# Kernel tuning notes

Measured on AMD Instinct MI355X. Metric: run time of the kernel, lower is better.

## Reference

```python
import jax, jax.numpy as jnp
import numpy as np

HEADS = 8
DIM_HEAD = 32
SCALE = DIM_HEAD ** -0.5


def _split_heads(t):
    # [b, n, h*d] -> [b, h, n, d]
    b, n, hd = t.shape
    return t.reshape(b, n, HEADS, hd // HEADS).transpose(0, 2, 1, 3)


def setup_inputs() -> dict:
    key = jax.random.key(0)
    k1, k2, k3, k4 = jax.random.split(key, 4)
    b, n, dim = 2, 2048, 256
    inner = HEADS * DIM_HEAD  # 256
    x = jax.random.normal(k1, (b, n, dim), dtype=jnp.float32)
    attn_feat = jax.random.normal(k2, (b, n, dim), dtype=jnp.float32)
    # nn.Linear(dim, 3*inner, bias=False): store as [dim, 3*inner] for x @ W
    W_qkv = jax.random.normal(k3, (dim, 3 * inner), dtype=jnp.float32) * (dim ** -0.5)
    W_qkv_aux = jax.random.normal(k4, (dim, 3 * inner), dtype=jnp.float32) * (dim ** -0.5)
    return {"x": x, "attn_feat": attn_feat, "W_qkv": W_qkv, "W_qkv_aux": W_qkv_aux,
            "use_cls_tokens": 1}


def reference(x, attn_feat, W_qkv, W_qkv_aux, use_cls_tokens):
    b, n, dim = x.shape
    # aux Q,K (v_aux computed but unused, matching original chunk of 3)
    qkv_aux = attn_feat @ W_qkv_aux            # [b, n, 3*inner]
    q_aux, k_aux, _ = jnp.split(qkv_aux, 3, axis=-1)
    q_aux, k_aux = _split_heads(q_aux), _split_heads(k_aux)
    # self Q,K
    qkv_self = x @ W_qkv
    q_self, k_self, _ = jnp.split(qkv_self, 3, axis=-1)
    q_self, k_self = _split_heads(q_self), _split_heads(k_self)
    # dual score product: (QK^T_aux * scale) * (QK^T_self * scale)
    dots_aux = jnp.einsum('bhid,bhjd->bhij', q_aux, k_aux) * SCALE
    dots_self = jnp.einsum('bhid,bhjd->bhij', q_self, k_self) * SCALE
    attn = jax.nn.softmax(dots_aux * dots_self, axis=-1)  # [b, h, n, n]
    # v = x.unsqueeze(1): broadcast raw x over heads
    out = jnp.einsum('bhij,bjd->bhid', attn, x)           # [b, h, n, dim]
    out = out.transpose(0, 2, 1, 3).reshape(b, n, HEADS * dim)
    attn_flat = attn.transpose(0, 2, 1, 3).reshape(b, n, HEADS * n)
    return (out, out[:, 0], attn_flat[:, 0])
```

## Files before the change

### kernel.cpp

```cpp
#include <hip/hip_runtime.h>

typedef _Float16 f16;
typedef _Float16 f16x4 __attribute__((ext_vector_type(4)));
typedef _Float16 f16x8 __attribute__((ext_vector_type(8)));
typedef float f32x4 __attribute__((ext_vector_type(4)));

#define LOG2E 1.4426950408889634f

__global__ __launch_bounds__(256) void k_transpose(const float* __restrict__ x,
                                                   f16* __restrict__ xt) {
  __shared__ f16 tile[64][65];
  int n0 = blockIdx.x * 64;
  int d0 = blockIdx.y * 64;
  int b  = blockIdx.z;
  int t = threadIdx.x;
  int colr = t & 63, rowg = t >> 6;
#pragma unroll
  for (int r = 0; r < 16; ++r) {
    int row = r * 4 + rowg;
    tile[row][colr] = (f16)x[(b * 2048 + n0 + row) * 256 + d0 + colr];
  }
  __syncthreads();
#pragma unroll
  for (int r = 0; r < 16; ++r) {
    int drow = r * 4 + rowg;
    xt[(b * 256 + d0 + drow) * 2048 + n0 + colr] = tile[colr][drow];
  }
}

__global__ __launch_bounds__(256) void k_proj(const float* __restrict__ x,
    const float* __restrict__ af, const float* __restrict__ Wq,
    const float* __restrict__ Wa, f16* __restrict__ Qs, f16* __restrict__ Ks,
    f16* __restrict__ Qa, f16* __restrict__ Ka) {
  __shared__ f16 Alds[64][264];
  __shared__ f16 Wlds[64][264];
  int mt = blockIdx.x, nt = blockIdx.y, s = blockIdx.z;
  const float* A = s ? af : x;
  const float* W = s ? Wa : Wq;
  f16* Qd = s ? Qa : Qs;
  f16* Kd = s ? Ka : Ks;
  int t = threadIdx.x;
  int m0 = mt * 64, n0 = nt * 64;
  {
    int row = t >> 2, cb = (t & 3) * 64;
    const float* src = A + (m0 + row) * 256 + cb;
#pragma unroll
    for (int r = 0; r < 16; ++r) {
      float4 v = *(const float4*)(src + r * 4);
      f16x4 hv = { (f16)v.x, (f16)v.y, (f16)v.z, (f16)v.w };
      *(f16x4*)&Alds[row][cb + r * 4] = hv;
    }
  }
  {
    int k0 = t >> 4, c4 = (t & 15) * 4;
#pragma unroll
    for (int r = 0; r < 16; ++r) {
      int k = k0 + r * 16;
      float4 v = *(const float4*)(W + k * 768 + n0 + c4);
      Wlds[c4 + 0][k] = (f16)v.x;
      Wlds[c4 + 1][k] = (f16)v.y;
      Wlds[c4 + 2][k] = (f16)v.z;
      Wlds[c4 + 3][k] = (f16)v.w;
    }
  }
  __syncthreads();
  int wv = t >> 6, ln = t & 63, cl = ln & 15, g = ln >> 4;
  f32x4 z4 = {0.f, 0.f, 0.f, 0.f};
  f32x4 acc[4] = {z4, z4, z4, z4};
#pragma unroll
  for (int k32 = 0; k32 < 8; ++k32) {
    f16x8 a = *(const f16x8*)&Alds[wv * 16 + cl][k32 * 32 + g * 8];
#pragma unroll
    for (int n4 = 0; n4 < 4; ++n4) {
      f16x8 bf = *(const f16x8*)&Wlds[n4 * 16 + cl][k32 * 32 + g * 8];
      acc[n4] = __builtin_amdgcn_mfma_f32_16x16x32_f16(a, bf, acc[n4], 0, 0, 0);
    }
  }
#pragma unroll
  for (int n4 = 0; n4 < 4; ++n4) {
    int c = n0 + n4 * 16 + cl;
    int head = (c & 255) >> 5, d = c & 31;
    f16* dst = (c < 256) ? Qd : Kd;
#pragma unroll
    for (int r = 0; r < 4; ++r) {
      int m = m0 + wv * 16 + g * 4 + r;
      int bb = m >> 11, nn = m & 2047;
      dst[((bb * 8 + head) * 2048 + nn) * 32 + d] = (f16)acc[n4][r];
    }
  }
}

__global__ __launch_bounds__(256, 2) void k_flash(const f16* __restrict__ Qs,
    const f16* __restrict__ Ks, const f16* __restrict__ Qa,
    const f16* __restrict__ Ka, const f16* __restrict__ xt,
    float* __restrict__ out, float* __restrict__ out_cls) {
  __shared__ f16 KaL[64][40];
  __shared__ f16 KsL[64][40];
  __shared__ f16 XtL[256][72];
  __shared__ f16 PL[4][16][72];
  int qt = blockIdx.x, h = blockIdx.y, b = blockIdx.z;
  int bh = b * 8 + h;
  int t = threadIdx.x, wv = t >> 6, ln = t & 63, cl = ln & 15, g = ln >> 4;
  int qrow0 = qt * 64 + wv * 16;
  f16x8 qsf = *(const f16x8*)&Qs[(bh * 2048 + qrow0 + cl) * 32 + g * 8];
  f16x8 qaf = *(const f16x8*)&Qa[(bh * 2048 + qrow0 + cl) * 32 + g * 8];
  f32x4 z4 = {0.f, 0.f, 0.f, 0.f};
  f32x4 acc[16];
#pragma unroll
  for (int i = 0; i < 16; ++i) acc[i] = z4;
  float m_run = -__builtin_inff(), l_run = 0.f;
  int krow = t >> 2, koff = (t & 3) * 8;
  const f16* kaSrc = Ka + (bh * 2048 + krow) * 32 + koff;
  const f16* ksSrc = Ks + (bh * 2048 + krow) * 32 + koff;
  const f16* xsrc = xt + (b * 256 + t) * 2048;

  for (int kt = 0; kt < 32; ++kt) {
    __syncthreads();
    *(f16x8*)&KaL[krow][koff] = *(const f16x8*)(kaSrc + kt * 64 * 32);
    *(f16x8*)&KsL[krow][koff] = *(const f16x8*)(ksSrc + kt * 64 * 32);
    {
      const f16* sx = xsrc + kt * 64;
      f16x8* drow = (f16x8*)&XtL[t][0];
#pragma unroll
      for (int r = 0; r < 8; ++r) drow[r] = *(const f16x8*)(sx + r * 8);
    }
    __syncthreads();
    float p[16];
    float tmax = -__builtin_inff();
#pragma unroll
    for (int jt = 0; jt < 4; ++jt) {
      f16x8 kaf = *(const f16x8*)&KaL[jt * 16 + cl][g * 8];
      f16x8 ksf = *(const f16x8*)&KsL[jt * 16 + cl][g * 8];
      f32x4 za = __builtin_amdgcn_mfma_f32_16x16x32_f16(kaf, qaf, z4, 0, 0, 0);
      f32x4 zs = __builtin_amdgcn_mfma_f32_16x16x32_f16(ksf, qsf, z4, 0, 0, 0);
#pragma unroll
      for (int r = 0; r < 4; ++r) {
        float sv = za[r] * zs[r] * (1.f / 32.f);
        p[jt * 4 + r] = sv;
        tmax = fmaxf(tmax, sv);
      }
    }
    tmax = fmaxf(tmax, __shfl_xor(tmax, 16, 64));
    tmax = fmaxf(tmax, __shfl_xor(tmax, 32, 64));
    float m_new = fmaxf(m_run, tmax);
    float alpha = exp2f((m_run - m_new) * LOG2E);
    float lsum = 0.f;
#pragma unroll
    for (int q = 0; q < 16; ++q) {
      p[q] = exp2f((p[q] - m_new) * LOG2E);
      lsum += p[q];
    }
    lsum += __shfl_xor(lsum, 16, 64);
    lsum += __shfl_xor(lsum, 32, 64);
    l_run = l_run * alpha + lsum;
    m_run = m_new;
    float af4[4];
#pragma unroll
    for (int r = 0; r < 4; ++r) af4[r] = __shfl(alpha, g * 4 + r, 64);
#pragma unroll
    for (int dt = 0; dt < 16; ++dt)
#pragma unroll
      for (int r = 0; r < 4; ++r) acc[dt][r] *= af4[r];
#pragma unroll
    for (int jt = 0; jt < 4; ++jt) {
      f16x4 pk = { (f16)p[jt * 4 + 0], (f16)p[jt * 4 + 1],
                   (f16)p[jt * 4 + 2], (f16)p[jt * 4 + 3] };
      *(f16x4*)&PL[wv][cl][jt * 16 + g * 4] = pk;
    }
#pragma unroll
    for (int k32 = 0; k32 < 2; ++k32) {
      f16x8 pf = *(const f16x8*)&PL[wv][cl][k32 * 32 + g * 8];
#pragma unroll
      for (int dt = 0; dt < 16; ++dt) {
        f16x8 xf = *(const f16x8*)&XtL[dt * 16 + cl][k32 * 32 + g * 8];
        acc[dt] = __builtin_amdgcn_mfma_f32_16x16x32_f16(pf, xf, acc[dt], 0, 0, 0);
      }
    }
  }
  float lf[4];
#pragma unroll
  for (int r = 0; r < 4; ++r) lf[r] = __shfl(l_run, g * 4 + r, 64);
#pragma unroll
  for (int dt = 0; dt < 16; ++dt) {
    int col = h * 256 + dt * 16 + cl;
#pragma unroll
    for (int r = 0; r < 4; ++r) {
      int qrow = qrow0 + g * 4 + r;
      float v = acc[dt][r] / lf[r];
      out[(b * 2048 + qrow) * 2048 + col] = v;
      if (qrow == 0) out_cls[b * 2048 + col] = v;
    }
  }
}

__global__ __launch_bounds__(256) void k_attn0(const f16* __restrict__ Qs,
    const f16* __restrict__ Ks, const f16* __restrict__ Qa,
    const f16* __restrict__ Ka, float* __restrict__ dst) {
  __shared__ float qa_s[32], qs_s[32];
  __shared__ float red[256];
  int h = blockIdx.x, b = blockIdx.y, bh = b * 8 + h;
  int t = threadIdx.x;
  if (t < 32) {
    qa_s[t] = (float)Qa[bh * 2048 * 32 + t];
    qs_s[t] = (float)Qs[bh * 2048 * 32 + t];
  }
  __syncthreads();
  float sv[8];
#pragma unroll
  for (int r = 0; r < 8; ++r) {
    int j = r * 256 + t;
    const f16x8* ka8 = (const f16x8*)&Ka[(bh * 2048 + j) * 32];
    const f16x8* ks8 = (const f16x8*)&Ks[(bh * 2048 + j) * 32];
    float da = 0.f, ds = 0.f;
#pragma unroll
    for (int c = 0; c < 4; ++c) {
      f16x8 va = ka8[c], vs = ks8[c];
#pragma unroll
      for (int d = 0; d < 8; ++d) {
        da += qa_s[c * 8 + d] * (float)va[d];
        ds += qs_s[c * 8 + d] * (float)vs[d];
      }
    }
    sv[r] = da * ds * (1.f / 32.f);
  }
  float mx = sv[0];
#pragma unroll
  for (int r = 1; r < 8; ++r) mx = fmaxf(mx, sv[r]);
  red[t] = mx;
  __syncthreads();
  for (int st = 128; st > 0; st >>= 1) {
    if (t < st) red[t] = fmaxf(red[t], red[t + st]);
    __syncthreads();
  }
  float m = red[0];
  __syncthreads();
  float e[8], sum = 0.f;
#pragma unroll
  for (int r = 0; r < 8; ++r) {
    e[r] = exp2f((sv[r] - m) * LOG2E);
    sum += e[r];
  }
  red[t] = sum;
  __syncthreads();
  for (int st = 128; st > 0; st >>= 1) {
    if (t < st) red[t] += red[t + st];
    __syncthreads();
  }
  float l = red[0];
#pragma unroll
  for (int r = 0; r < 8; ++r)
    dst[b * 16384 + h * 2048 + r * 256 + t] = e[r] / l;
}

extern "C" void kernel_launch(void* const* d_in, const int* in_sizes, int n_in,
                              void* d_out, int out_size, void* d_ws, size_t ws_size,
                              hipStream_t stream) {
  const float* x  = (const float*)d_in[0];
  const float* af = (const float*)d_in[1];
  const float* Wq = (const float*)d_in[2];
  const float* Wa = (const float*)d_in[3];
  const size_t QK = (size_t)2 * 8 * 2048 * 32;
  f16* Qs = (f16*)d_ws;
  f16* Ks = Qs + QK;
  f16* Qa = Ks + QK;
  f16* Ka = Qa + QK;
  f16* xt = Ka + QK;
  float* out     = (float*)d_out;
  float* out_cls = out + (size_t)2 * 2048 * 2048;
  float* attn0   = out_cls + 2 * 2048;

  k_transpose<<<dim3(32, 4, 2), 256, 0, stream>>>(x, xt);
  k_proj<<<dim3(64, 8, 2), 256, 0, stream>>>(x, af, Wq, Wa, Qs, Ks, Qa, Ka);
  k_flash<<<dim3(32, 8, 2), 256, 0, stream>>>(Qs, Ks, Qa, Ka, xt, out, out_cls);
  k_attn0<<<dim3(8, 2), 256, 0, stream>>>(Qs, Ks, Qa, Ka, attn0);
}
```

Measured before the change: 200.9 us.

## Restructure flash kernel to split output columns across waves and pre-transpose weights

The flash kernel no longer stages x^T in shared memory. Each wave now owns 64 output columns for all 64 query rows and loads its x^T fragments directly from global memory, with the probabilities shared through LDS. K tiles are double-buffered and prefetched, the log2e factor is folded into the score scale, and accumulator rescaling is skipped when no row max changed. The projection kernel reads a pre-transposed f16 weight produced by a new kernel, plus A straight from global, with no LDS staging. The trade is one extra launch and more global traffic per block for x^T, in exchange for less LDS use and fewer barriers.

```diff
diff --git a/kernel.cpp b/kernel.cpp
--- a/kernel.cpp
+++ b/kernel.cpp
@@ -6,6 +6,7 @@
 typedef float f32x4 __attribute__((ext_vector_type(4)));
 
 #define LOG2E 1.4426950408889634f
+#define SCL   (1.4426950408889634f / 32.0f)
 
 __global__ __launch_bounds__(256) void k_transpose(const float* __restrict__ x,
                                                    f16* __restrict__ xt) {
@@ -18,61 +19,60 @@
 #pragma unroll
   for (int r = 0; r < 16; ++r) {
     int row = r * 4 + rowg;
-    tile[row][colr] = (f16)x[(b * 2048 + n0 + row) * 256 + d0 + colr];
+    tile[row][colr] = (f16)x[((size_t)b * 2048 + n0 + row) * 256 + d0 + colr];
   }
   __syncthreads();
 #pragma unroll
   for (int r = 0; r < 16; ++r) {
     int drow = r * 4 + rowg;
-    xt[(b * 256 + d0 + drow) * 2048 + n0 + colr] = tile[colr][drow];
+    xt[((size_t)b * 256 + d0 + drow) * 2048 + n0 + colr] = tile[colr][drow];
+  }
+}
+
+__global__ __launch_bounds__(256) void k_transW(const float* __restrict__ Wq,
+    const float* __restrict__ Wa, f16* __restrict__ Wt) {
+  __shared__ f16 tile[64][65];
+  int n0 = blockIdx.x * 64, k0 = blockIdx.y * 64, s = blockIdx.z;
+  const float* W = s ? Wa : Wq;
+  f16* dst = Wt + (size_t)s * 512 * 256;
+  int t = threadIdx.x, c = t & 63, rg = t >> 6;
+#pragma unroll
+  for (int r = 0; r < 16; ++r) {
+    int krow = r * 4 + rg;
+    tile[krow][c] = (f16)W[(size_t)(k0 + krow) * 768 + n0 + c];
+  }
+  __syncthreads();
+#pragma unroll
+  for (int r = 0; r < 16; ++r) {
+    int nrow = r * 4 + rg;
+    dst[(size_t)(n0 + nrow) * 256 + k0 + c] = tile[c][nrow];
   }
 }
 
 __global__ __launch_bounds__(256) void k_proj(const float* __restrict__ x,
-    const float* __restrict__ af, const float* __restrict__ Wq,
-    const float* __restrict__ Wa, f16* __restrict__ Qs, f16* __restrict__ Ks,
+    const float* __restrict__ af, const f16* __restrict__ Wt,
+    f16* __restrict__ Qs, f16* __restrict__ Ks,
     f16* __restrict__ Qa, f16* __restrict__ Ka) {
-  __shared__ f16 Alds[64][264];
-  __shared__ f16 Wlds[64][264];
   int mt = blockIdx.x, nt = blockIdx.y, s = blockIdx.z;
   const float* A = s ? af : x;
-  const float* W = s ? Wa : Wq;
+  const f16* W = Wt + (size_t)s * 512 * 256;
   f16* Qd = s ? Qa : Qs;
   f16* Kd = s ? Ka : Ks;
-  int t = threadIdx.x;
+  int t = threadIdx.x, wv = t >> 6, ln = t & 63, cl = ln & 15, g = ln >> 4;
   int m0 = mt * 64, n0 = nt * 64;
-  {
-    int row = t >> 2, cb = (t & 3) * 64;
-    const float* src = A + (m0 + row) * 256 + cb;
-#pragma unroll
-    for (int r = 0; r < 16; ++r) {
-      float4 v = *(const float4*)(src + r * 4);
-      f16x4 hv = { (f16)v.x, (f16)v.y, (f16)v.z, (f16)v.w };
-      *(f16x4*)&Alds[row][cb + r * 4] = hv;
-    }
-  }
-  {
-    int k0 = t >> 4, c4 = (t & 15) * 4;
-#pragma unroll
-    for (int r = 0; r < 16; ++r) {
-      int k = k0 + r * 16;
-      float4 v = *(const float4*)(W + k * 768 + n0 + c4);
-      Wlds[c4 + 0][k] = (f16)v.x;
-      Wlds[c4 + 1][k] = (f16)v.y;
-      Wlds[c4 + 2][k] = (f16)v.z;
-      Wlds[c4 + 3][k] = (f16)v.w;
-    }
-  }
-  __syncthreads();
-  int wv = t >> 6, ln = t & 63, cl = ln & 15, g = ln >> 4;
+  const float* arow = A + (size_t)(m0 + wv * 16 + cl) * 256 + g * 8;
+  const f16* wb = W + (size_t)n0 * 256 + g * 8;
   f32x4 z4 = {0.f, 0.f, 0.f, 0.f};
   f32x4 acc[4] = {z4, z4, z4, z4};
 #pragma unroll
   for (int k32 = 0; k32 < 8; ++k32) {
-    f16x8 a = *(const f16x8*)&Alds[wv * 16 + cl][k32 * 32 + g * 8];
+    float4 u = *(const float4*)(arow + k32 * 32);
+    float4 v = *(const float4*)(arow + k32 * 32 + 4);
+    f16x8 a = { (f16)u.x, (f16)u.y, (f16)u.z, (f16)u.w,
+                (f16)v.x, (f16)v.y, (f16)v.z, (f16)v.w };
 #pragma unroll
     for (int n4 = 0; n4 < 4; ++n4) {
-      f16x8 bf = *(const f16x8*)&Wlds[n4 * 16 + cl][k32 * 32 + g * 8];
+      f16x8 bf = *(const f16x8*)(wb + (size_t)(n4 * 16 + cl) * 256 + k32 * 32);
       acc[n4] = __builtin_amdgcn_mfma_f32_16x16x32_f16(a, bf, acc[n4], 0, 0, 0);
     }
   }
@@ -85,57 +85,67 @@
     for (int r = 0; r < 4; ++r) {
       int m = m0 + wv * 16 + g * 4 + r;
       int bb = m >> 11, nn = m & 2047;
-      dst[((bb * 8 + head) * 2048 + nn) * 32 + d] = (f16)acc[n4][r];
-    }
-  }
-}
-
-__global__ __launch_bounds__(256, 2) void k_flash(const f16* __restrict__ Qs,
+      dst[(((size_t)bb * 8 + head) * 2048 + nn) * 32 + d] = (f16)acc[n4][r];
+    }
+  }
+}
+
+__global__ __launch_bounds__(256) void k_flash(const f16* __restrict__ Qs,
     const f16* __restrict__ Ks, const f16* __restrict__ Qa,
     const f16* __restrict__ Ka, const f16* __restrict__ xt,
     float* __restrict__ out, float* __restrict__ out_cls) {
-  __shared__ f16 KaL[64][40];
-  __shared__ f16 KsL[64][40];
-  __shared__ f16 XtL[256][72];
-  __shared__ f16 PL[4][16][72];
+  __shared__ f16 KaL[2][64][40];
+  __shared__ f16 KsL[2][64][40];
+  __shared__ f16 PL[2][64][72];
+  __shared__ float alphaL[2][64];
+  __shared__ float lL[64];
   int qt = blockIdx.x, h = blockIdx.y, b = blockIdx.z;
   int bh = b * 8 + h;
   int t = threadIdx.x, wv = t >> 6, ln = t & 63, cl = ln & 15, g = ln >> 4;
   int qrow0 = qt * 64 + wv * 16;
-  f16x8 qsf = *(const f16x8*)&Qs[(bh * 2048 + qrow0 + cl) * 32 + g * 8];
-  f16x8 qaf = *(const f16x8*)&Qa[(bh * 2048 + qrow0 + cl) * 32 + g * 8];
+  f16x8 qsf = *(const f16x8*)&Qs[((size_t)bh * 2048 + qrow0 + cl) * 32 + g * 8];
+  f16x8 qaf = *(const f16x8*)&Qa[((size_t)bh * 2048 + qrow0 + cl) * 32 + g * 8];
   f32x4 z4 = {0.f, 0.f, 0.f, 0.f};
-  f32x4 acc[16];
-#pragma unroll
-  for (int i = 0; i < 16; ++i) acc[i] = z4;
-  float m_run = -__builtin_inff(), l_run = 0.f;
+  f32x4 acc[4][4];
+#pragma unroll
+  for (int i = 0; i < 4; ++i)
+#pragma unroll
+    for (int j = 0; j < 4; ++j) acc[i][j] = z4;
+  float m_run = -3.0e38f, l_run = 0.f;
   int krow = t >> 2, koff = (t & 3) * 8;
-  const f16* kaSrc = Ka + (bh * 2048 + krow) * 32 + koff;
-  const f16* ksSrc = Ks + (bh * 2048 + krow) * 32 + koff;
-  const f16* xsrc = xt + (b * 256 + t) * 2048;
+  const f16* kaSrc = Ka + ((size_t)bh * 2048 + krow) * 32 + koff;
+  const f16* ksSrc = Ks + ((size_t)bh * 2048 + krow) * 32 + koff;
+  const f16* xb = xt + ((size_t)b * 256 + wv * 64) * 2048;
+
+  *(f16x8*)&KaL[0][krow][koff] = *(const f16x8*)kaSrc;
+  *(f16x8*)&KsL[0][krow][koff] = *(const f16x8*)ksSrc;
+  __syncthreads();
 
   for (int kt = 0; kt < 32; ++kt) {
-    __syncthreads();
-    *(f16x8*)&KaL[krow][koff] = *(const f16x8*)(kaSrc + kt * 64 * 32);
-    *(f16x8*)&KsL[krow][koff] = *(const f16x8*)(ksSrc + kt * 64 * 32);
-    {
-      const f16* sx = xsrc + kt * 64;
-      f16x8* drow = (f16x8*)&XtL[t][0];
-#pragma unroll
-      for (int r = 0; r < 8; ++r) drow[r] = *(const f16x8*)(sx + r * 8);
-    }
-    __syncthreads();
+    int buf = kt & 1;
+    f16x8 kan, ksn;
+    if (kt < 31) {
+      kan = *(const f16x8*)(kaSrc + (size_t)(kt + 1) * 2048);
+      ksn = *(const f16x8*)(ksSrc + (size_t)(kt + 1) * 2048);
+    }
+    f16x8 xf[2][4];
+#pragma unroll
+    for (int ks2 = 0; ks2 < 2; ++ks2)
+#pragma unroll
+      for (int ddt = 0; ddt < 4; ++ddt)
+        xf[ks2][ddt] = *(const f16x8*)(xb + (size_t)(ddt * 16 + cl) * 2048 +
+                                       kt * 64 + ks2 * 32 + g * 8);
     float p[16];
-    float tmax = -__builtin_inff();
+    float tmax = -3.0e38f;
 #pragma unroll
     for (int jt = 0; jt < 4; ++jt) {
-      f16x8 kaf = *(const f16x8*)&KaL[jt * 16 + cl][g * 8];
-      f16x8 ksf = *(const f16x8*)&KsL[jt * 16 + cl][g * 8];
+      f16x8 kaf = *(const f16x8*)&KaL[buf][jt * 16 + cl][g * 8];
+      f16x8 ksf = *(const f16x8*)&KsL[buf][jt * 16 + cl][g * 8];
       f32x4 za = __builtin_amdgcn_mfma_f32_16x16x32_f16(kaf, qaf, z4, 0, 0, 0);
       f32x4 zs = __builtin_amdgcn_mfma_f32_16x16x32_f16(ksf, qsf, z4, 0, 0, 0);
 #pragma unroll
       for (int r = 0; r < 4; ++r) {
-        float sv = za[r] * zs[r] * (1.f / 32.f);
+        float sv = za[r] * zs[r] * SCL;
         p[jt * 4 + r] = sv;
         tmax = fmaxf(tmax, sv);
       }
@@ -143,52 +153,76 @@
     tmax = fmaxf(tmax, __shfl_xor(tmax, 16, 64));
     tmax = fmaxf(tmax, __shfl_xor(tmax, 32, 64));
     float m_new = fmaxf(m_run, tmax);
-    float alpha = exp2f((m_run - m_new) * LOG2E);
+    float alpha = exp2f(m_run - m_new);
     float lsum = 0.f;
 #pragma unroll
     for (int q = 0; q < 16; ++q) {
-      p[q] = exp2f((p[q] - m_new) * LOG2E);
+      p[q] = exp2f(p[q] - m_new);
       lsum += p[q];
     }
     lsum += __shfl_xor(lsum, 16, 64);
     lsum += __shfl_xor(lsum, 32, 64);
     l_run = l_run * alpha + lsum;
     m_run = m_new;
-    float af4[4];
-#pragma unroll
-    for (int r = 0; r < 4; ++r) af4[r] = __shfl(alpha, g * 4 + r, 64);
-#pragma unroll
-    for (int dt = 0; dt < 16; ++dt)
-#pragma unroll
-      for (int r = 0; r < 4; ++r) acc[dt][r] *= af4[r];
+    if (kt < 31) {
+      *(f16x8*)&KaL[buf ^ 1][krow][koff] = kan;
+      *(f16x8*)&KsL[buf ^ 1][krow][koff] = ksn;
+    }
 #pragma unroll
     for (int jt = 0; jt < 4; ++jt) {
       f16x4 pk = { (f16)p[jt * 4 + 0], (f16)p[jt * 4 + 1],
                    (f16)p[jt * 4 + 2], (f16)p[jt * 4 + 3] };
-      *(f16x4*)&PL[wv][cl][jt * 16 + g * 4] = pk;
-    }
-#pragma unroll
-    for (int k32 = 0; k32 < 2; ++k32) {
-      f16x8 pf = *(const f16x8*)&PL[wv][cl][k32 * 32 + g * 8];
-#pragma unroll
-      for (int dt = 0; dt < 16; ++dt) {
-        f16x8 xf = *(const f16x8*)&XtL[dt * 16 + cl][k32 * 32 + g * 8];
-        acc[dt] = __builtin_amdgcn_mfma_f32_16x16x32_f16(pf, xf, acc[dt], 0, 0, 0);
+      *(f16x4*)&PL[buf][wv * 16 + cl][jt * 16 + g * 4] = pk;
+    }
+    if (g == 0) alphaL[buf][wv * 16 + cl] = alpha;
+    __syncthreads();
+    float av[4][4];
+    int need = 0;
+#pragma unroll
+    for (int qt2 = 0; qt2 < 4; ++qt2)
+#pragma unroll
+      for (int r = 0; r < 4; ++r) {
+        float a = alphaL[buf][qt2 * 16 + g * 4 + r];
+        av[qt2][r] = a;
+        need |= (a != 1.0f);
       }
-    }
-  }
-  float lf[4];
-#pragma unroll
-  for (int r = 0; r < 4; ++r) lf[r] = __shfl(l_run, g * 4 + r, 64);
-#pragma unroll
-  for (int dt = 0; dt < 16; ++dt) {
-    int col = h * 256 + dt * 16 + cl;
+    if (__any(need)) {
+#pragma unroll
+      for (int qt2 = 0; qt2 < 4; ++qt2)
+#pragma unroll
+        for (int ddt = 0; ddt < 4; ++ddt)
+#pragma unroll
+          for (int r = 0; r < 4; ++r) acc[qt2][ddt][r] *= av[qt2][r];
+    }
+#pragma unroll
+    for (int ks2 = 0; ks2 < 2; ++ks2) {
+      f16x8 pf[4];
+#pragma unroll
+      for (int qt2 = 0; qt2 < 4; ++qt2)
+        pf[qt2] = *(const f16x8*)&PL[buf][qt2 * 16 + cl][ks2 * 32 + g * 8];
+#pragma unroll
+      for (int ddt = 0; ddt < 4; ++ddt)
+#pragma unroll
+        for (int qt2 = 0; qt2 < 4; ++qt2)
+          acc[qt2][ddt] = __builtin_amdgcn_mfma_f32_16x16x32_f16(
+              pf[qt2], xf[ks2][ddt], acc[qt2][ddt], 0, 0, 0);
+    }
+  }
+  if (g == 0) lL[wv * 16 + cl] = l_run;
+  __syncthreads();
+#pragma unroll
+  for (int qt2 = 0; qt2 < 4; ++qt2) {
 #pragma unroll
     for (int r = 0; r < 4; ++r) {
-      int qrow = qrow0 + g * 4 + r;
-      float v = acc[dt][r] / lf[r];
-      out[(b * 2048 + qrow) * 2048 + col] = v;
-      if (qrow == 0) out_cls[b * 2048 + col] = v;
+      float linv = 1.0f / lL[qt2 * 16 + g * 4 + r];
+      int q = qt * 64 + qt2 * 16 + g * 4 + r;
+#pragma unroll
+      for (int ddt = 0; ddt < 4; ++ddt) {
+        float v = acc[qt2][ddt][r] * linv;
+        int col = h * 256 + wv * 64 + ddt * 16 + cl;
+        out[((size_t)b * 2048 + q) * 2048 + col] = v;
+        if (q == 0) out_cls[(size_t)b * 2048 + col] = v;
+      }
     }
   }
 }
@@ -201,16 +235,16 @@
   int h = blockIdx.x, b = blockIdx.y, bh = b * 8 + h;
   int t = threadIdx.x;
   if (t < 32) {
-    qa_s[t] = (float)Qa[bh * 2048 * 32 + t];
-    qs_s[t] = (float)Qs[bh * 2048 * 32 + t];
+    qa_s[t] = (float)Qa[(size_t)bh * 2048 * 32 + t];
+    qs_s[t] = (float)Qs[(size_t)bh * 2048 * 32 + t];
   }
   __syncthreads();
   float sv[8];
 #pragma unroll
   for (int r = 0; r < 8; ++r) {
     int j = r * 256 + t;
-    const f16x8* ka8 = (const f16x8*)&Ka[(bh * 2048 + j) * 32];
-    const f16x8* ks8 = (const f16x8*)&Ks[(bh * 2048 + j) * 32];
+    const f16x8* ka8 = (const f16x8*)&Ka[((size_t)bh * 2048 + j) * 32];
+    const f16x8* ks8 = (const f16x8*)&Ks[((size_t)bh * 2048 + j) * 32];
     float da = 0.f, ds = 0.f;
 #pragma unroll
     for (int c = 0; c < 4; ++c) {
@@ -249,7 +283,7 @@
   float l = red[0];
 #pragma unroll
   for (int r = 0; r < 8; ++r)
-    dst[b * 16384 + h * 2048 + r * 256 + t] = e[r] / l;
+    dst[(size_t)b * 16384 + h * 2048 + r * 256 + t] = e[r] / l;
 }
 
 extern "C" void kernel_launch(void* const* d_in, const int* in_sizes, int n_in,
@@ -265,12 +299,14 @@
   f16* Qa = Ks + QK;
   f16* Ka = Qa + QK;
   f16* xt = Ka + QK;
+  f16* Wt = xt + QK;
   float* out     = (float*)d_out;
   float* out_cls = out + (size_t)2 * 2048 * 2048;
   float* attn0   = out_cls + 2 * 2048;
 
   k_transpose<<<dim3(32, 4, 2), 256, 0, stream>>>(x, xt);
-  k_proj<<<dim3(64, 8, 2), 256, 0, stream>>>(x, af, Wq, Wa, Qs, Ks, Qa, Ka);
+  k_transW<<<dim3(8, 4, 2), 256, 0, stream>>>(Wq, Wa, Wt);
+  k_proj<<<dim3(64, 8, 2), 256, 0, stream>>>(x, af, Wt, Qs, Ks, Qa, Ka);
   k_flash<<<dim3(32, 8, 2), 256, 0, stream>>>(Qs, Ks, Qa, Ka, xt, out, out_cls);
   k_attn0<<<dim3(8, 2), 256, 0, stream>>>(Qs, Ks, Qa, Ka, attn0);
 }
```

Result: faster. 187.8 us (-6.5%).
